# Optimization experiments

Hardware: AMD Instinct MI355X
Metric: run time of the kernel (lower is better)

Reference implementation:

```python
import jax, jax.numpy as jnp
import numpy as np

N, HID, K = 256, 64, 2
B, T_ENC, T_DEC = 64, 12, 12
IN_DIM, OUT_DIM = 2, 1
NUM_SUPPORTS = 2
M = NUM_SUPPORTS * K + 1  # identity + K hops per support


def setup_inputs() -> dict:
    key = jax.random.key(0)
    ks = jax.random.split(key, 16)

    def w(k, shape, scale=0.05):
        return jax.random.normal(k, shape, dtype=jnp.float32) * scale

    def support(k):
        S = jax.random.uniform(k, (N, N), dtype=jnp.float32)
        return S / jnp.sum(S, axis=1, keepdims=True)  # random-walk normalized

    F0e = IN_DIM + HID   # encoder layer-0 concat(input, hidden) feature dim
    F1 = HID + HID       # layer-1 feature dim
    F0d = OUT_DIM + HID  # decoder layer-0 feature dim
    return {
        "encoder_inputs": jax.random.normal(ks[0], (B, T_ENC, N, IN_DIM), dtype=jnp.float32),
        "decoder_inputs": jax.random.normal(ks[1], (B, T_DEC, N, OUT_DIM), dtype=jnp.float32),
        "support0": support(ks[2]),
        "support1": support(ks[3]),
        "enc0_Wg": w(ks[4], (F0e, M, 2 * HID)), "enc0_bg": jnp.ones((2 * HID,), jnp.float32),
        "enc0_Wc": w(ks[5], (F0e, M, HID)),     "enc0_bc": jnp.zeros((HID,), jnp.float32),
        "enc1_Wg": w(ks[6], (F1, M, 2 * HID)),  "enc1_bg": jnp.ones((2 * HID,), jnp.float32),
        "enc1_Wc": w(ks[7], (F1, M, HID)),      "enc1_bc": jnp.zeros((HID,), jnp.float32),
        "dec0_Wg": w(ks[8], (F0d, M, 2 * HID)), "dec0_bg": jnp.ones((2 * HID,), jnp.float32),
        "dec0_Wc": w(ks[9], (F0d, M, HID)),     "dec0_bc": jnp.zeros((HID,), jnp.float32),
        "dec1_Wg": w(ks[10], (F1, M, 2 * HID)), "dec1_bg": jnp.ones((2 * HID,), jnp.float32),
        "dec1_Wc": w(ks[11], (F1, M, HID)),     "dec1_bc": jnp.zeros((HID,), jnp.float32),
        "proj_W": w(ks[12], (HID, OUT_DIM), 0.1),
        "proj_b": jnp.zeros((OUT_DIM,), jnp.float32),
    }


def _diff_conv(supports, x, h, W, b, in_dim):
    # x: (B, N*in_dim), h: (B, N*HID), W: (F, M, O) matching torch flatten order (f*M+m)
    Bsz = x.shape[0]
    xs = jnp.concatenate([x.reshape(Bsz, N, in_dim), h.reshape(Bsz, N, HID)], axis=-1)
    mats = [xs]
    for S in supports:
        x0 = xs
        x1 = jnp.einsum('mn,bnf->bmf', S, xs)
        mats.append(x1)
        for _ in range(2, K + 1):
            x2 = 2.0 * jnp.einsum('mn,bnf->bmf', S, x1) - x0  # Chebyshev recurrence
            mats.append(x2)
            x1, x0 = x2, x1
    X = jnp.stack(mats, axis=2)  # (B, N, M, F)
    out = jnp.einsum('bnmf,fmo->bno', X, W) + b
    return out.reshape(Bsz, -1)


def _cell(supports, x, h, Wg, bg, Wc, bc, in_dim):
    # DCGRUCell: sigmoid gates from diffusion conv, tanh candidate, GRU update
    Bsz = x.shape[0]
    ru = jax.nn.sigmoid(_diff_conv(supports, x, h, Wg, bg, in_dim)).reshape(Bsz, N, 2 * HID)
    r = ru[..., :HID].reshape(Bsz, N * HID)
    u = ru[..., HID:].reshape(Bsz, N * HID)
    c = jnp.tanh(_diff_conv(supports, x, r * h, Wc, bc, in_dim))
    return u * h + (1.0 - u) * c


def _forward(encoder_inputs, decoder_inputs, support0, support1,
             enc0_Wg, enc0_bg, enc0_Wc, enc0_bc, enc1_Wg, enc1_bg, enc1_Wc, enc1_bc,
             dec0_Wg, dec0_bg, dec0_Wc, dec0_bc, dec1_Wg, dec1_bg, dec1_Wc, dec1_bc,
             proj_W, proj_b):
    sup = (support0, support1)
    Bsz = encoder_inputs.shape[0]
    # encoder: (B,T,N,D) -> (T,B,N*D); zero initial hidden
    cur = jnp.transpose(encoder_inputs, (1, 0, 2, 3)).reshape(T_ENC, Bsz, N * IN_DIM)
    enc_params = [(enc0_Wg, enc0_bg, enc0_Wc, enc0_bc, IN_DIM),
                  (enc1_Wg, enc1_bg, enc1_Wc, enc1_bc, HID)]
    h_enc = []
    for (Wg, bg, Wc, bc, ind) in enc_params:
        h0 = jnp.zeros((Bsz, N * HID), cur.dtype)
        def estep(h, x, Wg=Wg, bg=bg, Wc=Wc, bc=bc, ind=ind):
            hn = _cell(sup, x, h, Wg, bg, Wc, bc, ind)
            return hn, hn
        hT, cur = jax.lax.scan(estep, h0, cur)
        h_enc.append(hT)
    # decoder (eval mode: no teacher forcing, dropout off); go symbol = zeros
    dec_params = [(dec0_Wg, dec0_bg, dec0_Wc, dec0_bc, OUT_DIM),
                  (dec1_Wg, dec1_bg, dec1_Wc, dec1_bc, HID)]
    go = jnp.zeros((Bsz, N * OUT_DIM), cur.dtype)

    def dstep(carry, _):
        hs, cur_in = carry
        out = cur_in
        new_hs = []
        for i, (Wg, bg, Wc, bc, ind) in enumerate(dec_params):
            hn = _cell(sup, out, hs[i], Wg, bg, Wc, bc, ind)
            out = hn
            new_hs.append(hn)
        proj = (jnp.einsum('bnh,ho->bno', out.reshape(Bsz, N, HID), proj_W) + proj_b)
        proj = proj.reshape(Bsz, N * OUT_DIM)
        return ((new_hs[0], new_hs[1]), proj), proj

    _, outs = jax.lax.scan(dstep, ((h_enc[0], h_enc[1]), go), None, length=T_DEC)
    outs = outs.reshape(T_DEC, Bsz, N, OUT_DIM)
    return jnp.transpose(outs, (1, 0, 2, 3))  # (B, T_DEC, N, OUT_DIM)


def reference(encoder_inputs, decoder_inputs, support0, support1,
              enc0_Wg, enc0_bg, enc0_Wc, enc0_bc, enc1_Wg, enc1_bg, enc1_Wc, enc1_bc,
              dec0_Wg, dec0_bg, dec0_Wc, dec0_bc, dec1_Wg, dec1_bg, dec1_Wc, dec1_bc,
              proj_W, proj_b):
    return _forward(encoder_inputs, decoder_inputs, support0, support1,
                    enc0_Wg, enc0_bg, enc0_Wc, enc0_bc, enc1_Wg, enc1_bg, enc1_Wc, enc1_bc,
                    dec0_Wg, dec0_bg, dec0_Wc, dec0_bc, dec1_Wg, dec1_bg, dec1_Wc, dec1_bc,
                    proj_W, proj_b)
```

## Files before the change

kernel.cpp:

```cpp
#include <hip/hip_runtime.h>
#include <stdint.h>


typedef short short8 __attribute__((ext_vector_type(8)));
typedef float f32x4 __attribute__((ext_vector_type(4)));
typedef unsigned short ushort4v __attribute__((ext_vector_type(4)));
typedef unsigned long long u64;
typedef int i32x4 __attribute__((ext_vector_type(4)));

#define DEVI __device__ __forceinline__

DEVI unsigned short f2bf(float x) {
  unsigned int u = __builtin_bit_cast(unsigned int, x);
  u += 0x7FFFu + ((u >> 16) & 1u);
  return (unsigned short)(u >> 16);
}
DEVI void ast(u64* p, u64 v) { __hip_atomic_store(p, v, __ATOMIC_RELAXED, __HIP_MEMORY_SCOPE_AGENT); }
DEVI float aldf(const float* p) { return __hip_atomic_load(p, __ATOMIC_RELAXED, __HIP_MEMORY_SCOPE_AGENT); }
DEVI void astf(float* p, float v) { __hip_atomic_store(p, v, __ATOMIC_RELAXED, __HIP_MEMORY_SCOPE_AGENT); }

DEVI i32x4 ldg_sc01(const void* p) {
  i32x4 r;
  asm volatile("global_load_dwordx4 %0, %1, off sc0 sc1" : "=v"(r) : "v"(p));
  return r;
}

struct KP {
  const float* enc_in;
  const float* sup0; const float* sup1;
  const float* Wsrc[8];
  const float* bias[8];
  const float* prW; const float* prB;
  float* out;
  unsigned short* A;
  unsigned short* Wp[8];
  unsigned short* H0[2];
  unsigned short* H1[2];
  unsigned short* RH0;
  unsigned short* RH1;
  float* XD;
  unsigned* ctr;
};

__global__ void prep(KP p) {
  const int i = blockIdx.x, tid = threadIdx.x;
  {
    const int s = i & 1, r = i >> 1;
    const float* S = s ? p.sup1 : p.sup0;
    float acc = 0.f;
    for (int k = 0; k < 256; ++k) acc = fmaf(S[r * 256 + k], S[k * 256 + tid], acc);
    p.A[(2 * s + 0) * 65536 + r * 256 + tid] = f2bf(S[r * 256 + tid]);
    p.A[(2 * s + 1) * 65536 + r * 256 + tid] = f2bf(2.f * acc - (r == tid ? 1.f : 0.f));
  }
  {
    const int gtid = i * 256 + tid;
    const int Fs[8]  = {66, 66, 128, 128, 65, 65, 128, 128};
    const int Os[8]  = {128, 64, 128, 64, 128, 64, 128, 64};
    const int FPs[8] = {96, 96, 128, 128, 96, 96, 128, 128};
    for (int w = 0; w < 8; ++w) {
      const int FPw = FPs[w], KPw = 5 * FPw, tot = Os[w] * KPw;
      for (int e = gtid; e < tot; e += 512 * 256) {
        const int o = e / KPw, k2 = e - o * KPw, m = k2 / FPw, f = k2 - m * FPw;
        p.Wp[w][e] = f2bf((f < Fs[w]) ? p.Wsrc[w][(f * 5 + m) * Os[w] + o] : 0.f);
      }
    }
  }
  {
    const int gtid = i * 256 + tid;
    u64* z0 = (u64*)p.H0[0];
    u64* z1 = (u64*)p.H1[0];
    ast(z0 + 2 * gtid, 0); ast(z0 + 2 * gtid + 1, 0);
    ast(z1 + 2 * gtid, 0); ast(z1 + 2 * gtid + 1, 0);
  }
  if (i == 0 && tid < 64)
    __hip_atomic_store(p.ctr + tid * 64, 0u, __ATOMIC_RELAXED, __HIP_MEMORY_SCOPE_AGENT);
}

template<int IND, int FP, int MODE>
DEVI void dc_stage(int b, int n0, int tid,
                   const float* xf32,
                   const unsigned short* xbf,
                   const unsigned short* hrows,
                   const unsigned short* Amats,
                   const unsigned short* Wp, const float* bias,
                   f32x4 (&hreg)[2], f32x4 (&ureg)[2],
                   unsigned short* grows,
                   const float* projW, const float* projB,
                   float* outp, float* xdout,
                   unsigned short* xsT, unsigned short* Hbuf)
{
  constexpr int F = IND + 64;
  constexpr int O = (MODE == 0) ? 128 : 64;
  constexpr int KPW = 5 * FP;
  constexpr int XS = 264;
  constexpr int HS = 136;
  constexpr int HB = 64 * HS;
  constexpr int NFT = FP / 16;
  constexpr int NOT_ = O / 16;
  constexpr int FT_W = (NFT + 3) / 4;
  constexpr int OT_W = (NOT_ + 3) / 4;

  const int wv8 = tid >> 6, ln = tid & 63;
  const int l15 = ln & 15, l4 = ln >> 4;
  const int wr = wv8 & 1, wc = wv8 >> 1;
  const int r0 = wr * 32;

  {
    i32x4 va[4];
#pragma unroll
    for (int it = 0; it < 4; ++it)
      va[it] = ldg_sc01(reinterpret_cast<const char*>(hrows) + (tid + it * 512) * 16);
    i32x4 vb[4];
    if (IND == 64) {
#pragma unroll
      for (int it = 0; it < 4; ++it)
        vb[it] = ldg_sc01(reinterpret_cast<const char*>(xbf) + (tid + it * 512) * 16);
    }
    asm volatile("s_waitcnt vmcnt(0)" ::: "memory");
#pragma unroll
    for (int it = 0; it < 4; ++it) {
      const int g = tid + it * 512, row = g >> 5, c = g & 31;
      *reinterpret_cast<i32x4*>(&xsT[(IND + row) * XS + c * 8]) = va[it];
    }
    if (IND == 64) {
#pragma unroll
      for (int it = 0; it < 4; ++it) {
        const int g = tid + it * 512, row = g >> 5, c = g & 31;
        *reinterpret_cast<i32x4*>(&xsT[row * XS + c * 8]) = vb[it];
      }
    }
  }
  if (IND == 2) {
    const float v = xf32[tid];
    xsT[(tid & 1) * XS + (tid >> 1)] = f2bf(v);
  } else if (IND == 1) {
    if (tid < 256) xsT[tid] = xf32 ? f2bf(aldf(xf32 + tid)) : (unsigned short)0;
  }
  if (F < FP) {
    for (int e = tid; e < (FP - F) * 256; e += 512)
      xsT[(F + (e >> 8)) * XS + (e & 255)] = 0;
  }
  __syncthreads();
#pragma unroll
  for (int it = 0; it < FP / 8; ++it) {
    const int e = tid + it * 512, f = e >> 6, nl = e & 63;
    Hbuf[nl * HS + f] = xsT[f * XS + n0 + nl];
  }
  __syncthreads();

  f32x4 pacc[2][OT_W];
#pragma unroll
  for (int rt = 0; rt < 2; ++rt)
#pragma unroll
    for (int oi = 0; oi < OT_W; ++oi) pacc[rt][oi] = 0.f;

  auto proj_step = [&](int m, const unsigned short* hb) {
#pragma unroll
    for (int k0 = 0; k0 < FP; k0 += 32) {
      short8 af[2];
#pragma unroll
      for (int rt = 0; rt < 2; ++rt)
        af[rt] = *reinterpret_cast<const short8*>(&hb[(r0 + rt * 16 + l15) * HS + k0 + l4 * 8]);
#pragma unroll
      for (int oi = 0; oi < OT_W; ++oi) {
        const int ot = wc + 4 * oi;
        if (ot < NOT_) {
          short8 bf = *reinterpret_cast<const short8*>(&Wp[(ot * 16 + l15) * KPW + m * FP + k0 + l4 * 8]);
#pragma unroll
          for (int rt = 0; rt < 2; ++rt)
            pacc[rt][oi] = __builtin_amdgcn_mfma_f32_16x16x32_bf16(af[rt], bf, pacc[rt][oi], 0, 0, 0);
        }
      }
    }
  };

  proj_step(0, Hbuf);

  for (int mi = 0; mi < 4; ++mi) {
    const unsigned short* Am = Amats + mi * 65536;
    f32x4 hacc[2][FT_W];
#pragma unroll
    for (int rt = 0; rt < 2; ++rt)
#pragma unroll
      for (int fi = 0; fi < FT_W; ++fi) hacc[rt][fi] = 0.f;

#pragma unroll
    for (int k0 = 0; k0 < 256; k0 += 32) {
      short8 af[2];
#pragma unroll
      for (int rt = 0; rt < 2; ++rt)
        af[rt] = *reinterpret_cast<const short8*>(&Am[(n0 + r0 + rt * 16 + l15) * 256 + k0 + l4 * 8]);
#pragma unroll
      for (int fi = 0; fi < FT_W; ++fi) {
        const int ft = wc + 4 * fi;
        if (ft < NFT) {
          short8 bf = *reinterpret_cast<const short8*>(&xsT[(ft * 16 + l15) * XS + k0 + l4 * 8]);
#pragma unroll
          for (int rt = 0; rt < 2; ++rt)
            hacc[rt][fi] = __builtin_amdgcn_mfma_f32_16x16x32_bf16(af[rt], bf, hacc[rt][fi], 0, 0, 0);
        }
      }
    }
    unsigned short* dst = Hbuf + ((mi + 1) & 1) * HB;
#pragma unroll
    for (int fi = 0; fi < FT_W; ++fi) {
      const int ft = wc + 4 * fi;
      if (ft < NFT) {
#pragma unroll
        for (int rt = 0; rt < 2; ++rt)
#pragma unroll
          for (int j = 0; j < 4; ++j)
            dst[(r0 + rt * 16 + l4 * 4 + j) * HS + ft * 16 + l15] = f2bf(hacc[rt][fi][j]);
      }
    }
    __syncthreads();
    proj_step(mi + 1, dst);
  }

  if (MODE == 0) {
    const float br = bias[wc * 16 + l15];
    const float bu = bias[64 + wc * 16 + l15];
#pragma unroll
    for (int rt = 0; rt < 2; ++rt) {
      f32x4 uu;
      ushort4v pk;
#pragma unroll
      for (int jj = 0; jj < 4; ++jj) {
        const float r = 1.f / (1.f + __expf(-(pacc[rt][0][jj] + br)));
        uu[jj] = 1.f / (1.f + __expf(-(pacc[rt][1][jj] + bu)));
        pk[jj] = f2bf(r * hreg[rt][jj]);
      }
      ureg[rt] = uu;
      ast((u64*)(grows + (wc * 16 + l15) * 256 + n0 + r0 + rt * 16 + l4 * 4),
          __builtin_bit_cast(u64, pk));
    }
  } else {
    float* hrow = reinterpret_cast<float*>(Hbuf);
    if (MODE == 2) __syncthreads();
    const float bc = bias[wc * 16 + l15];
#pragma unroll
    for (int rt = 0; rt < 2; ++rt) {
      f32x4 hn;
      ushort4v pk;
#pragma unroll
      for (int jj = 0; jj < 4; ++jj) {
        const float ex = __expf(2.f * (pacc[rt][0][jj] + bc));
        const float c = 1.f - 2.f / (ex + 1.f);
        hn[jj] = ureg[rt][jj] * hreg[rt][jj] + (1.f - ureg[rt][jj]) * c;
        pk[jj] = f2bf(hn[jj]);
      }
      hreg[rt] = hn;
      ast((u64*)(grows + (wc * 16 + l15) * 256 + n0 + r0 + rt * 16 + l4 * 4),
          __builtin_bit_cast(u64, pk));
      if (MODE == 2) {
#pragma unroll
        for (int jj = 0; jj < 4; ++jj)
          hrow[(r0 + rt * 16 + l4 * 4 + jj) * 68 + wc * 16 + l15] = hn[jj];
      }
    }
    if (MODE == 2) {
      __syncthreads();
      if (tid < 64) {
        float acc = projB[0];
        const float* hr = hrow + tid * 68;
#pragma unroll
        for (int hid = 0; hid < 64; ++hid) acc = fmaf(hr[hid], projW[hid], acc);
        outp[b * 3072 + n0 + tid] = acc;
        astf(xdout + b * 256 + n0 + tid, acc);
      }
    }
  }
}

__launch_bounds__(512, 2)
__global__ void dcrnn_main(KP p) {
  __shared__ __align__(16) unsigned short xsT[128 * 264];
  __shared__ __align__(16) unsigned short Hbuf[2 * 64 * 136];
  const int tid = threadIdx.x;
  const int i = (int)blockIdx.x;
  const int q = (i >> 3) & 3;
  const int b = (i & 7) + 8 * (i >> 5);
  const int n0 = q * 64;

  unsigned* ctr = p.ctr + b * 64;
  unsigned st = 0;
  auto BAR = [&]() {
    ++st;
    asm volatile("s_waitcnt vmcnt(0)" ::: "memory");
    __syncthreads();
    if (tid == 0) {
      __hip_atomic_fetch_add(ctr, 1u, __ATOMIC_RELAXED, __HIP_MEMORY_SCOPE_AGENT);
      const unsigned target = st * 4u;
      while (__hip_atomic_load(ctr, __ATOMIC_RELAXED, __HIP_MEMORY_SCOPE_AGENT) < target)
        __builtin_amdgcn_s_sleep(2);
    }
    __syncthreads();
  };

  f32x4 h0[2], h1[2], u[2];
#pragma unroll
  for (int rt = 0; rt < 2; ++rt) { h0[rt] = 0.f; h1[rt] = 0.f; u[rt] = 0.f; }
  int c0 = 0, c1 = 0;

  for (int t = 0; t < 12; ++t) {
    const float* x0 = p.enc_in + (b * 12 + t) * 512;
    dc_stage<2, 96, 0>(b, n0, tid, x0, nullptr, p.H0[c0] + b * 16384, p.A, p.Wp[0], p.bias[0],
                       h0, u, p.RH0 + b * 16384, nullptr, nullptr, nullptr, nullptr, xsT, Hbuf);
    BAR();
    dc_stage<2, 96, 1>(b, n0, tid, x0, nullptr, p.RH0 + b * 16384, p.A, p.Wp[1], p.bias[1],
                       h0, u, p.H0[c0 ^ 1] + b * 16384, nullptr, nullptr, nullptr, nullptr, xsT, Hbuf);
    BAR(); c0 ^= 1;
    dc_stage<64, 128, 0>(b, n0, tid, nullptr, p.H0[c0] + b * 16384, p.H1[c1] + b * 16384, p.A, p.Wp[2], p.bias[2],
                         h1, u, p.RH1 + b * 16384, nullptr, nullptr, nullptr, nullptr, xsT, Hbuf);
    BAR();
    dc_stage<64, 128, 1>(b, n0, tid, nullptr, p.H0[c0] + b * 16384, p.RH1 + b * 16384, p.A, p.Wp[3], p.bias[3],
                         h1, u, p.H1[c1 ^ 1] + b * 16384, nullptr, nullptr, nullptr, nullptr, xsT, Hbuf);
    BAR(); c1 ^= 1;
  }

  for (int t = 0; t < 12; ++t) {
    const float* xd = t ? (p.XD + b * 256) : nullptr;
    dc_stage<1, 96, 0>(b, n0, tid, xd, nullptr, p.H0[c0] + b * 16384, p.A, p.Wp[4], p.bias[4],
                       h0, u, p.RH0 + b * 16384, nullptr, nullptr, nullptr, nullptr, xsT, Hbuf);
    BAR();
    dc_stage<1, 96, 1>(b, n0, tid, xd, nullptr, p.RH0 + b * 16384, p.A, p.Wp[5], p.bias[5],
                       h0, u, p.H0[c0 ^ 1] + b * 16384, nullptr, nullptr, nullptr, nullptr, xsT, Hbuf);
    BAR(); c0 ^= 1;
    dc_stage<64, 128, 0>(b, n0, tid, nullptr, p.H0[c0] + b * 16384, p.H1[c1] + b * 16384, p.A, p.Wp[6], p.bias[6],
                         h1, u, p.RH1 + b * 16384, nullptr, nullptr, nullptr, nullptr, xsT, Hbuf);
    BAR();
    dc_stage<64, 128, 2>(b, n0, tid, nullptr, p.H0[c0] + b * 16384, p.RH1 + b * 16384, p.A, p.Wp[7], p.bias[7],
                         h1, u, p.H1[c1 ^ 1] + b * 16384, p.prW, p.prB, p.out + t * 256, p.XD, xsT, Hbuf);
    if (t != 11) BAR();
    c1 ^= 1;
  }
}

extern "C" void kernel_launch(void* const* d_in, const int* in_sizes, int n_in,
                              void* d_out, int out_size, void* d_ws, size_t ws_size,
                              hipStream_t stream)
{
  (void)in_sizes; (void)n_in; (void)out_size; (void)ws_size;
  KP p;
  p.enc_in = (const float*)d_in[0];
  p.sup0 = (const float*)d_in[2];
  p.sup1 = (const float*)d_in[3];
  p.Wsrc[0] = (const float*)d_in[4];  p.bias[0] = (const float*)d_in[5];
  p.Wsrc[1] = (const float*)d_in[6];  p.bias[1] = (const float*)d_in[7];
  p.Wsrc[2] = (const float*)d_in[8];  p.bias[2] = (const float*)d_in[9];
  p.Wsrc[3] = (const float*)d_in[10]; p.bias[3] = (const float*)d_in[11];
  p.Wsrc[4] = (const float*)d_in[12]; p.bias[4] = (const float*)d_in[13];
  p.Wsrc[5] = (const float*)d_in[14]; p.bias[5] = (const float*)d_in[15];
  p.Wsrc[6] = (const float*)d_in[16]; p.bias[6] = (const float*)d_in[17];
  p.Wsrc[7] = (const float*)d_in[18]; p.bias[7] = (const float*)d_in[19];
  p.prW = (const float*)d_in[20];
  p.prB = (const float*)d_in[21];
  p.out = (float*)d_out;

  char* ws = (char*)d_ws;
  size_t off = 0;
  auto carve = [&](size_t bytes) -> char* {
    char* qp = ws + off;
    off += (bytes + 255) & ~(size_t)255;
    return qp;
  };
  p.A = (unsigned short*)carve(4 * 65536 * 2);
  p.Wp[0] = (unsigned short*)carve(128 * 480 * 2);
  p.Wp[1] = (unsigned short*)carve(64 * 480 * 2);
  p.Wp[2] = (unsigned short*)carve(128 * 640 * 2);
  p.Wp[3] = (unsigned short*)carve(64 * 640 * 2);
  p.Wp[4] = (unsigned short*)carve(128 * 480 * 2);
  p.Wp[5] = (unsigned short*)carve(64 * 480 * 2);
  p.Wp[6] = (unsigned short*)carve(128 * 640 * 2);
  p.Wp[7] = (unsigned short*)carve(64 * 640 * 2);
  p.H0[0] = (unsigned short*)carve(64 * 64 * 256 * 2);
  p.H0[1] = (unsigned short*)carve(64 * 64 * 256 * 2);
  p.H1[0] = (unsigned short*)carve(64 * 64 * 256 * 2);
  p.H1[1] = (unsigned short*)carve(64 * 64 * 256 * 2);
  p.RH0 = (unsigned short*)carve(64 * 64 * 256 * 2);
  p.RH1 = (unsigned short*)carve(64 * 64 * 256 * 2);
  p.XD = (float*)carve(64 * 256 * 4);
  p.ctr = (unsigned*)carve(64 * 256);

  prep<<<dim3(512), dim3(256), 0, stream>>>(p);
  dcrnn_main<<<dim3(256), dim3(512), 0, stream>>>(p);
}
```

Measured before the change: 2.736 ms.

## Split inter-block barrier to overlap identity-term projection with barrier wait

Replaces the combined arrive-and-wait barrier with a split one. Each stage now arrives at the end and waits only after computing the identity (m=0) projection from register-held local state (h, r*h, x), so that MFMA work overlaps the cross-block wait. The r*h product is kept in registers for this, and shared buffers are zeroed once at kernel start. Global loads drop the sc1 cache bit. The cost is more live registers and more complex synchronisation invariants.

```diff
diff --git a/kernel.cpp b/kernel.cpp
--- a/kernel.cpp
+++ b/kernel.cpp
@@ -19,9 +19,9 @@
 DEVI float aldf(const float* p) { return __hip_atomic_load(p, __ATOMIC_RELAXED, __HIP_MEMORY_SCOPE_AGENT); }
 DEVI void astf(float* p, float v) { __hip_atomic_store(p, v, __ATOMIC_RELAXED, __HIP_MEMORY_SCOPE_AGENT); }
 
-DEVI i32x4 ldg_sc01(const void* p) {
+DEVI i32x4 ldg_sc0(const void* p) {
   i32x4 r;
-  asm volatile("global_load_dwordx4 %0, %1, off sc0 sc1" : "=v"(r) : "v"(p));
+  asm volatile("global_load_dwordx4 %0, %1, off sc0" : "=v"(r) : "v"(p));
   return r;
 }
 
@@ -81,13 +81,15 @@
                    const float* xf32,
                    const unsigned short* xbf,
                    const unsigned short* hrows,
+                   f32x4 (&idh)[2], f32x4 (&idx)[2],
+                   f32x4 (&hreg)[2], f32x4 (&ureg)[2], f32x4 (&rhreg)[2],
                    const unsigned short* Amats,
                    const unsigned short* Wp, const float* bias,
-                   f32x4 (&hreg)[2], f32x4 (&ureg)[2],
                    unsigned short* grows,
                    const float* projW, const float* projB,
                    float* outp, float* xdout,
-                   unsigned short* xsT, unsigned short* Hbuf)
+                   unsigned short* xsT, unsigned short* Hbuf,
+                   unsigned* ctr, unsigned& st)
 {
   constexpr int F = IND + 64;
   constexpr int O = (MODE == 0) ? 128 : 64;
@@ -105,46 +107,26 @@
   const int wr = wv8 & 1, wc = wv8 >> 1;
   const int r0 = wr * 32;
 
-  {
-    i32x4 va[4];
-#pragma unroll
-    for (int it = 0; it < 4; ++it)
-      va[it] = ldg_sc01(reinterpret_cast<const char*>(hrows) + (tid + it * 512) * 16);
-    i32x4 vb[4];
-    if (IND == 64) {
-#pragma unroll
-      for (int it = 0; it < 4; ++it)
-        vb[it] = ldg_sc01(reinterpret_cast<const char*>(xbf) + (tid + it * 512) * 16);
-    }
-    asm volatile("s_waitcnt vmcnt(0)" ::: "memory");
-#pragma unroll
-    for (int it = 0; it < 4; ++it) {
-      const int g = tid + it * 512, row = g >> 5, c = g & 31;
-      *reinterpret_cast<i32x4*>(&xsT[(IND + row) * XS + c * 8]) = va[it];
-    }
-    if (IND == 64) {
-#pragma unroll
-      for (int it = 0; it < 4; ++it) {
-        const int g = tid + it * 512, row = g >> 5, c = g & 31;
-        *reinterpret_cast<i32x4*>(&xsT[row * XS + c * 8]) = vb[it];
-      }
-    }
-  }
+#pragma unroll
+  for (int rt = 0; rt < 2; ++rt)
+#pragma unroll
+    for (int j = 0; j < 4; ++j) {
+      const int nl = r0 + rt * 16 + l4 * 4 + j;
+      Hbuf[nl * HS + IND + wc * 16 + l15] = f2bf(idh[rt][j]);
+      if (IND == 64) Hbuf[nl * HS + wc * 16 + l15] = f2bf(idx[rt][j]);
+    }
   if (IND == 2) {
-    const float v = xf32[tid];
-    xsT[(tid & 1) * XS + (tid >> 1)] = f2bf(v);
+    if (tid < 128)
+      Hbuf[(tid >> 1) * HS + (tid & 1)] = f2bf(xf32[(n0 + (tid >> 1)) * 2 + (tid & 1)]);
   } else if (IND == 1) {
-    if (tid < 256) xsT[tid] = xf32 ? f2bf(aldf(xf32 + tid)) : (unsigned short)0;
+    if (tid < 64)
+      Hbuf[tid * HS] = xf32 ? f2bf(aldf(xf32 + n0 + tid)) : (unsigned short)0;
   }
   if (F < FP) {
-    for (int e = tid; e < (FP - F) * 256; e += 512)
-      xsT[(F + (e >> 8)) * XS + (e & 255)] = 0;
-  }
-  __syncthreads();
-#pragma unroll
-  for (int it = 0; it < FP / 8; ++it) {
-    const int e = tid + it * 512, f = e >> 6, nl = e & 63;
-    Hbuf[nl * HS + f] = xsT[f * XS + n0 + nl];
+    for (int e = tid; e < (FP - F) * 64; e += 512) {
+      const int f = F + (e >> 6), nl = e & 63;
+      Hbuf[nl * HS + f] = 0;
+    }
   }
   __syncthreads();
 
@@ -176,6 +158,45 @@
 
   proj_step(0, Hbuf);
 
+  if (tid == 0) {
+    const unsigned target = st * 4u;
+    while (__hip_atomic_load(ctr, __ATOMIC_RELAXED, __HIP_MEMORY_SCOPE_AGENT) < target)
+      __builtin_amdgcn_s_sleep(2);
+  }
+  __syncthreads();
+
+  {
+    i32x4 va[4];
+#pragma unroll
+    for (int it = 0; it < 4; ++it)
+      va[it] = ldg_sc0(reinterpret_cast<const char*>(hrows) + (tid + it * 512) * 16);
+    i32x4 vb[4];
+    if (IND == 64) {
+#pragma unroll
+      for (int it = 0; it < 4; ++it)
+        vb[it] = ldg_sc0(reinterpret_cast<const char*>(xbf) + (tid + it * 512) * 16);
+    }
+    asm volatile("s_waitcnt vmcnt(0)" ::: "memory");
+#pragma unroll
+    for (int it = 0; it < 4; ++it) {
+      const int g = tid + it * 512, row = g >> 5, c = g & 31;
+      *reinterpret_cast<i32x4*>(&xsT[(IND + row) * XS + c * 8]) = va[it];
+    }
+    if (IND == 64) {
+#pragma unroll
+      for (int it = 0; it < 4; ++it) {
+        const int g = tid + it * 512, row = g >> 5, c = g & 31;
+        *reinterpret_cast<i32x4*>(&xsT[row * XS + c * 8]) = vb[it];
+      }
+    }
+    if (IND == 2) {
+      xsT[(tid & 1) * XS + (tid >> 1)] = f2bf(xf32[tid]);
+    } else if (IND == 1) {
+      if (tid < 256) xsT[tid] = xf32 ? f2bf(aldf(xf32 + tid)) : (unsigned short)0;
+    }
+  }
+  __syncthreads();
+
   for (int mi = 0; mi < 4; ++mi) {
     const unsigned short* Am = Amats + mi * 65536;
     f32x4 hacc[2][FT_W];
@@ -222,15 +243,14 @@
     const float bu = bias[64 + wc * 16 + l15];
 #pragma unroll
     for (int rt = 0; rt < 2; ++rt) {
-      f32x4 uu;
       ushort4v pk;
 #pragma unroll
       for (int jj = 0; jj < 4; ++jj) {
         const float r = 1.f / (1.f + __expf(-(pacc[rt][0][jj] + br)));
-        uu[jj] = 1.f / (1.f + __expf(-(pacc[rt][1][jj] + bu)));
-        pk[jj] = f2bf(r * hreg[rt][jj]);
-      }
-      ureg[rt] = uu;
+        ureg[rt][jj] = 1.f / (1.f + __expf(-(pacc[rt][1][jj] + bu)));
+        rhreg[rt][jj] = r * hreg[rt][jj];
+        pk[jj] = f2bf(rhreg[rt][jj]);
+      }
       ast((u64*)(grows + (wc * 16 + l15) * 256 + n0 + r0 + rt * 16 + l4 * 4),
           __builtin_bit_cast(u64, pk));
     }
@@ -270,6 +290,11 @@
       }
     }
   }
+
+  asm volatile("s_waitcnt vmcnt(0)" ::: "memory");
+  __syncthreads();
+  if (tid == 0) __hip_atomic_fetch_add(ctr, 1u, __ATOMIC_RELAXED, __HIP_MEMORY_SCOPE_AGENT);
+  ++st;
 }
 
 __launch_bounds__(512, 2)
@@ -282,56 +307,62 @@
   const int b = (i & 7) + 8 * (i >> 5);
   const int n0 = q * 64;
 
+  for (int e = tid; e < 128 * 264; e += 512) xsT[e] = 0;
+  for (int e = tid; e < 2 * 64 * 136; e += 512) Hbuf[e] = 0;
+
   unsigned* ctr = p.ctr + b * 64;
   unsigned st = 0;
-  auto BAR = [&]() {
-    ++st;
-    asm volatile("s_waitcnt vmcnt(0)" ::: "memory");
-    __syncthreads();
-    if (tid == 0) {
-      __hip_atomic_fetch_add(ctr, 1u, __ATOMIC_RELAXED, __HIP_MEMORY_SCOPE_AGENT);
-      const unsigned target = st * 4u;
-      while (__hip_atomic_load(ctr, __ATOMIC_RELAXED, __HIP_MEMORY_SCOPE_AGENT) < target)
-        __builtin_amdgcn_s_sleep(2);
-    }
-    __syncthreads();
-  };
-
-  f32x4 h0[2], h1[2], u[2];
-#pragma unroll
-  for (int rt = 0; rt < 2; ++rt) { h0[rt] = 0.f; h1[rt] = 0.f; u[rt] = 0.f; }
+
+  __syncthreads();
+  if (tid == 0) __hip_atomic_fetch_add(ctr, 1u, __ATOMIC_RELAXED, __HIP_MEMORY_SCOPE_AGENT);
+  ++st;
+
+  f32x4 h0[2], h1[2], u[2], rh[2];
+#pragma unroll
+  for (int rt = 0; rt < 2; ++rt) { h0[rt] = 0.f; h1[rt] = 0.f; u[rt] = 0.f; rh[rt] = 0.f; }
   int c0 = 0, c1 = 0;
 
   for (int t = 0; t < 12; ++t) {
     const float* x0 = p.enc_in + (b * 12 + t) * 512;
-    dc_stage<2, 96, 0>(b, n0, tid, x0, nullptr, p.H0[c0] + b * 16384, p.A, p.Wp[0], p.bias[0],
-                       h0, u, p.RH0 + b * 16384, nullptr, nullptr, nullptr, nullptr, xsT, Hbuf);
-    BAR();
-    dc_stage<2, 96, 1>(b, n0, tid, x0, nullptr, p.RH0 + b * 16384, p.A, p.Wp[1], p.bias[1],
-                       h0, u, p.H0[c0 ^ 1] + b * 16384, nullptr, nullptr, nullptr, nullptr, xsT, Hbuf);
-    BAR(); c0 ^= 1;
-    dc_stage<64, 128, 0>(b, n0, tid, nullptr, p.H0[c0] + b * 16384, p.H1[c1] + b * 16384, p.A, p.Wp[2], p.bias[2],
-                         h1, u, p.RH1 + b * 16384, nullptr, nullptr, nullptr, nullptr, xsT, Hbuf);
-    BAR();
-    dc_stage<64, 128, 1>(b, n0, tid, nullptr, p.H0[c0] + b * 16384, p.RH1 + b * 16384, p.A, p.Wp[3], p.bias[3],
-                         h1, u, p.H1[c1 ^ 1] + b * 16384, nullptr, nullptr, nullptr, nullptr, xsT, Hbuf);
-    BAR(); c1 ^= 1;
+    dc_stage<2, 96, 0>(b, n0, tid, x0, nullptr, p.H0[c0] + b * 16384,
+                       h0, h0, h0, u, rh, p.A, p.Wp[0], p.bias[0],
+                       p.RH0 + b * 16384, nullptr, nullptr, nullptr, nullptr,
+                       xsT, Hbuf, ctr, st);
+    dc_stage<2, 96, 1>(b, n0, tid, x0, nullptr, p.RH0 + b * 16384,
+                       rh, h0, h0, u, rh, p.A, p.Wp[1], p.bias[1],
+                       p.H0[c0 ^ 1] + b * 16384, nullptr, nullptr, nullptr, nullptr,
+                       xsT, Hbuf, ctr, st);
+    c0 ^= 1;
+    dc_stage<64, 128, 0>(b, n0, tid, nullptr, p.H0[c0] + b * 16384, p.H1[c1] + b * 16384,
+                         h1, h0, h1, u, rh, p.A, p.Wp[2], p.bias[2],
+                         p.RH1 + b * 16384, nullptr, nullptr, nullptr, nullptr,
+                         xsT, Hbuf, ctr, st);
+    dc_stage<64, 128, 1>(b, n0, tid, nullptr, p.H0[c0] + b * 16384, p.RH1 + b * 16384,
+                         rh, h0, h1, u, rh, p.A, p.Wp[3], p.bias[3],
+                         p.H1[c1 ^ 1] + b * 16384, nullptr, nullptr, nullptr, nullptr,
+                         xsT, Hbuf, ctr, st);
+    c1 ^= 1;
   }
 
   for (int t = 0; t < 12; ++t) {
     const float* xd = t ? (p.XD + b * 256) : nullptr;
-    dc_stage<1, 96, 0>(b, n0, tid, xd, nullptr, p.H0[c0] + b * 16384, p.A, p.Wp[4], p.bias[4],
-                       h0, u, p.RH0 + b * 16384, nullptr, nullptr, nullptr, nullptr, xsT, Hbuf);
-    BAR();
-    dc_stage<1, 96, 1>(b, n0, tid, xd, nullptr, p.RH0 + b * 16384, p.A, p.Wp[5], p.bias[5],
-                       h0, u, p.H0[c0 ^ 1] + b * 16384, nullptr, nullptr, nullptr, nullptr, xsT, Hbuf);
-    BAR(); c0 ^= 1;
-    dc_stage<64, 128, 0>(b, n0, tid, nullptr, p.H0[c0] + b * 16384, p.H1[c1] + b * 16384, p.A, p.Wp[6], p.bias[6],
-                         h1, u, p.RH1 + b * 16384, nullptr, nullptr, nullptr, nullptr, xsT, Hbuf);
-    BAR();
-    dc_stage<64, 128, 2>(b, n0, tid, nullptr, p.H0[c0] + b * 16384, p.RH1 + b * 16384, p.A, p.Wp[7], p.bias[7],
-                         h1, u, p.H1[c1 ^ 1] + b * 16384, p.prW, p.prB, p.out + t * 256, p.XD, xsT, Hbuf);
-    if (t != 11) BAR();
+    dc_stage<1, 96, 0>(b, n0, tid, xd, nullptr, p.H0[c0] + b * 16384,
+                       h0, h0, h0, u, rh, p.A, p.Wp[4], p.bias[4],
+                       p.RH0 + b * 16384, nullptr, nullptr, nullptr, nullptr,
+                       xsT, Hbuf, ctr, st);
+    dc_stage<1, 96, 1>(b, n0, tid, xd, nullptr, p.RH0 + b * 16384,
+                       rh, h0, h0, u, rh, p.A, p.Wp[5], p.bias[5],
+                       p.H0[c0 ^ 1] + b * 16384, nullptr, nullptr, nullptr, nullptr,
+                       xsT, Hbuf, ctr, st);
+    c0 ^= 1;
+    dc_stage<64, 128, 0>(b, n0, tid, nullptr, p.H0[c0] + b * 16384, p.H1[c1] + b * 16384,
+                         h1, h0, h1, u, rh, p.A, p.Wp[6], p.bias[6],
+                         p.RH1 + b * 16384, nullptr, nullptr, nullptr, nullptr,
+                         xsT, Hbuf, ctr, st);
+    dc_stage<64, 128, 2>(b, n0, tid, nullptr, p.H0[c0] + b * 16384, p.RH1 + b * 16384,
+                         rh, h0, h1, u, rh, p.A, p.Wp[7], p.bias[7],
+                         p.H1[c1 ^ 1] + b * 16384, p.prW, p.prB,
+                         p.out + t * 256, p.XD, xsT, Hbuf, ctr, st);
     c1 ^= 1;
   }
 }
```

Measured after the change: 2.781 ms. Within noise of the previous version (+1.6%).
